# Kernel tuning notes

Measured on AMD Instinct MI355X. Metric: run time of the kernel, lower is better.

## Reference

```python
import math
import jax, jax.numpy as jnp
import numpy as np

H = 8  # num_heads

def _layernorm(x, scale, bias, eps=1e-5):
    m = x.mean(-1, keepdims=True)
    v = x.var(-1, keepdims=True)
    return (x - m) / jnp.sqrt(v + eps) * scale + bias

def setup_inputs() -> dict:
    key = jax.random.key(0)
    ks = jax.random.split(key, 12)
    B, C, P, D, G = 8, 32, 256, 256, 512
    n = jax.random.normal
    return {
        "qz": n(ks[0], (B, C, P, D), dtype=jnp.float32),
        "unary": n(ks[1], (B, C, P, D), dtype=jnp.float32),
        # per-sample condition-instantiated factors; scaled ~1/sqrt(D) so attn logits are sane
        "time_u": n(ks[2], (B, D, D), dtype=jnp.float32) * 0.06,
        "time_v": n(ks[3], (B, D, D), dtype=jnp.float32) * 0.06,
        "channel_u": n(ks[4], (B, D, D), dtype=jnp.float32) * 0.06,
        "channel_v": n(ks[5], (B, D, D), dtype=jnp.float32) * 0.06,
        "topic_binary": n(ks[6], (B, G, D), dtype=jnp.float32) * 0.02,
        "norm_scale": jnp.ones((D,), jnp.float32),
        "norm_bias": jnp.zeros((D,), jnp.float32),
        "gate_w": n(ks[7], (D, D), dtype=jnp.float32) * 0.02,
        "gate_b": jnp.zeros((D,), jnp.float32),
        "out_w1": n(ks[8], (D, D), dtype=jnp.float32) * 0.02,
        "out_b1": jnp.zeros((D,), jnp.float32),
        "out_w2": n(ks[9], (D, D), dtype=jnp.float32) * 0.02,
        "out_b2": jnp.zeros((D,), jnp.float32),
    }

def reference(qz, unary, time_u, time_v, channel_u, channel_v, topic_binary,
              norm_scale, norm_bias, gate_w, gate_b, out_w1, out_b1, out_w2, out_b2):
    B, C, P, D = qz.shape
    R = D // H
    inv_sqrt_r = 1.0 / math.sqrt(R)

    qz_n = _layernorm(qz, norm_scale, norm_bias)

    def heads(x, w):  # [B,C,P,D] x [B,D,D] -> [B,C,P,H,R]
        return jnp.einsum('bcpd,bod->bcpo', x, w).reshape(B, C, P, H, R)

    # --- time-factor message: attention over P within each (b, c, h) ---
    qu = heads(qz_n, time_u).transpose(0, 1, 3, 2, 4)   # [B,C,H,P,R]
    qv = heads(qz_n, time_v).transpose(0, 1, 3, 2, 4)
    attn_t = jax.nn.softmax(jnp.einsum('bchpr,bchqr->bchpq', qu, qv) * inv_sqrt_r, axis=-1)
    m_t = jnp.einsum('bchpq,bcqd->bchpd', attn_t, qz_n).mean(axis=2)  # [B,C,P,D]

    # --- channel-factor message: attention over C within each (b, p, h) ---
    qu = heads(qz_n, channel_u).transpose(0, 2, 3, 1, 4)  # [B,P,H,C,R]
    qv = heads(qz_n, channel_v).transpose(0, 2, 3, 1, 4)
    attn_c = jax.nn.softmax(jnp.einsum('bphcr,bphfr->bphcf', qu, qv) * inv_sqrt_r, axis=-1)
    qzp = qz_n.transpose(0, 2, 1, 3)                      # [B,P,C,D]
    m_c = jnp.einsum('bphcf,bpfd->bphcd', attn_c, qzp).mean(axis=2).transpose(0, 2, 1, 3)

    # --- topic-modeling binary factor with AbsNormalize (relu + L1-normalize) ---
    qg = jax.nn.relu(jnp.einsum('bcpd,bgd->bcpg', qz_n, topic_binary))
    qg = qg / jnp.maximum(qg.sum(axis=-1, keepdims=True), 1e-6)
    m_g = jnp.einsum('bcpg,bgd->bcpd', qg, topic_binary)

    # --- gated residual update ---
    gate = jax.nn.sigmoid(qz @ gate_w.T + gate_b)
    qz2 = gate * qz + (1.0 - gate) * (unary + m_t + m_c + m_g)

    # --- output MLP with shared LayerNorm ---
    h = _layernorm(qz2, norm_scale, norm_bias)
    h = jax.nn.gelu(h @ out_w1.T + out_b1, approximate=False) @ out_w2.T + out_b2
    return qz2 + h
```

## Files before the change

### kernel.cpp

```cpp
#include <hip/hip_runtime.h>
#include <math.h>

namespace {

constexpr float INV_SQRT_R = 0.17677669529663689f;

typedef __attribute__((ext_vector_type(8))) __bf16 bf16x8;
typedef __attribute__((ext_vector_type(4))) float f32x4;

static __device__ __forceinline__ f32x4 MF(bf16x8 a, bf16x8 b, f32x4 c) {
    return __builtin_amdgcn_mfma_f32_16x16x32_bf16(a, b, c, 0, 0, 0);
}

__global__ __launch_bounds__(256) void prep_kernel(
    const float* __restrict__ time_u, const float* __restrict__ time_v,
    const float* __restrict__ chan_u, const float* __restrict__ chan_v,
    const float* __restrict__ topic, const float* __restrict__ gate_w,
    const float* __restrict__ w1, const float* __restrict__ w2,
    __bf16* __restrict__ wtime, __bf16* __restrict__ wchan,
    __bf16* __restrict__ topicb, __bf16* __restrict__ topicTb,
    __bf16* __restrict__ gwb, __bf16* __restrict__ w1b, __bf16* __restrict__ w2b)
{
    __shared__ __bf16 tile[32][34];
    const int blk = blockIdx.x;
    const int t = threadIdx.x;
    if (blk < 2048) {
        const int q = blk >> 9, r = blk & 511;
        const float* src; __bf16* dst; int dstOff;
        if (q == 0)      { src = time_u; dst = wtime; dstOff = 0; }
        else if (q == 1) { src = time_v; dst = wtime; dstOff = 65536; }
        else if (q == 2) { src = chan_u; dst = wchan; dstOff = 0; }
        else             { src = chan_v; dst = wchan; dstOff = 65536; }
        int i = (r * 256 + t) * 4;
        float4 v = *(const float4*)(src + i);
        int o = (i >> 16) * 131072 + dstOff + (i & 65535);
        dst[o + 0] = (__bf16)v.x; dst[o + 1] = (__bf16)v.y;
        dst[o + 2] = (__bf16)v.z; dst[o + 3] = (__bf16)v.w;
    } else if (blk < 3072) {
        int i = ((blk - 2048) * 256 + t) * 4;
        float4 v = *(const float4*)(topic + i);
        topicb[i + 0] = (__bf16)v.x; topicb[i + 1] = (__bf16)v.y;
        topicb[i + 2] = (__bf16)v.z; topicb[i + 3] = (__bf16)v.w;
    } else if (blk < 4096) {
        const int idx = blk - 3072;
        const int r0 = (idx & 15) * 32;
        const int c0 = ((idx >> 4) & 7) * 32;
        const size_t bz = idx >> 7;
        const float* src = topic + bz * 131072;
        __bf16* dst = topicTb + bz * 131072;
        const int tx = t & 31, ty = t >> 5;
        #pragma unroll
        for (int i = 0; i < 32; i += 8)
            tile[ty + i][tx] = (__bf16)src[(size_t)(r0 + ty + i) * 256 + c0 + tx];
        __syncthreads();
        #pragma unroll
        for (int i = 0; i < 32; i += 8)
            dst[(size_t)(c0 + ty + i) * 512 + r0 + tx] = tile[tx][ty + i];
    } else {
        const int w = (blk - 4096) >> 6;
        const int r = (blk - 4096) & 63;
        const float* src = (w == 0) ? gate_w : ((w == 1) ? w1 : w2);
        __bf16* dst = (w == 0) ? gwb : ((w == 1) ? w1b : w2b);
        int i = (r * 256 + t) * 4;
        float4 v = *(const float4*)(src + i);
        dst[i + 0] = (__bf16)v.x; dst[i + 1] = (__bf16)v.y;
        dst[i + 2] = (__bf16)v.z; dst[i + 3] = (__bf16)v.w;
    }
}

__global__ __launch_bounds__(256) void ln_kernel(
    const float* __restrict__ x, const float* __restrict__ sc,
    const float* __restrict__ bi, __bf16* __restrict__ y)
{
    const size_t row = blockIdx.x;
    const int t = threadIdx.x;
    const float v = x[row * 256 + t];
    float s = v, s2 = v * v;
    #pragma unroll
    for (int o = 32; o > 0; o >>= 1) {
        s  += __shfl_xor(s, o);
        s2 += __shfl_xor(s2, o);
    }
    __shared__ float ps[4], ps2[4];
    if ((t & 63) == 0) { ps[t >> 6] = s; ps2[t >> 6] = s2; }
    __syncthreads();
    const float S  = ps[0] + ps[1] + ps[2] + ps[3];
    const float S2 = ps2[0] + ps2[1] + ps2[2] + ps2[3];
    const float mean = S * (1.0f / 256.0f);
    const float var  = S2 * (1.0f / 256.0f) - mean * mean;
    const float inv  = 1.0f / sqrtf(var + 1e-5f);
    y[row * 256 + t] = (__bf16)((v - mean) * inv * sc[t] + bi[t]);
}

__global__ __launch_bounds__(256) void tpose_bf_kernel(
    const __bf16* __restrict__ src, __bf16* __restrict__ dst, int R, int C)
{
    const size_t bz = blockIdx.z;
    src += bz * (size_t)R * C;
    dst += bz * (size_t)R * C;
    __shared__ __bf16 tile[32][34];
    const int r0 = blockIdx.x * 32, c0 = blockIdx.y * 32;
    const int tx = threadIdx.x & 31, ty = threadIdx.x >> 5;
    #pragma unroll
    for (int i = 0; i < 32; i += 8)
        tile[ty + i][tx] = src[(size_t)(r0 + ty + i) * C + c0 + tx];
    __syncthreads();
    #pragma unroll
    for (int i = 0; i < 32; i += 8)
        dst[(size_t)(c0 + ty + i) * R + r0 + tx] = tile[tx][ty + i];
}

__global__ __launch_bounds__(256) void mgemm_kernel(
    const __bf16* __restrict__ A, const __bf16* __restrict__ Bm, __bf16* __restrict__ Cout,
    int K, size_t aStride, size_t bStride,
    size_t s_b, size_t s_c, size_t s_p, size_t s_w, size_t s_h)
{
    const int bb = blockIdx.z;
    const int m0 = blockIdx.x * 64;
    const int n0 = blockIdx.y * 256;
    const __bf16* Ab = A + (size_t)bb * aStride;
    const __bf16* Bb = Bm + (size_t)bb * bStride;
    __shared__ __align__(16) __bf16 As[64][40];
    __shared__ __align__(16) __bf16 Bs[256][40];
    const int t = threadIdx.x;
    const int lane = t & 63;
    const int wid = t >> 6;
    const int l15 = lane & 15, lg = lane >> 4;

    f32x4 acc[4][4] = {};

    for (int k0 = 0; k0 < K; k0 += 32) {
        {
            const int row = t >> 2, k8 = (t & 3) << 3;
            *(bf16x8*)&As[row][k8] = *(const bf16x8*)(Ab + (size_t)(m0 + row) * K + k0 + k8);
        }
        #pragma unroll
        for (int s = 0; s < 4; ++s) {
            const int slot = s * 256 + t;
            const int row = slot >> 2, k8 = (slot & 3) << 3;
            *(bf16x8*)&Bs[row][k8] = *(const bf16x8*)(Bb + (size_t)(n0 + row) * K + k0 + k8);
        }
        __syncthreads();
        bf16x8 af[4], bfr[4];
        #pragma unroll
        for (int i = 0; i < 4; ++i)
            af[i] = *(const bf16x8*)&As[i * 16 + l15][lg * 8];
        #pragma unroll
        for (int j = 0; j < 4; ++j)
            bfr[j] = *(const bf16x8*)&Bs[wid * 64 + j * 16 + l15][lg * 8];
        #pragma unroll
        for (int i = 0; i < 4; ++i)
            #pragma unroll
            for (int j = 0; j < 4; ++j)
                acc[i][j] = MF(af[i], bfr[j], acc[i][j]);
        __syncthreads();
    }

    #pragma unroll
    for (int j = 0; j < 4; ++j) {
        const int n = n0 + wid * 64 + j * 16 + l15;
        const size_t offn = (size_t)(n >> 8) * s_w + (size_t)((n >> 5) & 7) * s_h + (n & 31);
        #pragma unroll
        for (int i = 0; i < 4; ++i) {
            #pragma unroll
            for (int r = 0; r < 4; ++r) {
                const int m = m0 + i * 16 + lg * 4 + r;
                const size_t off = (size_t)bb * s_b + (size_t)(m >> 8) * s_c
                                 + (size_t)(m & 255) * s_p + offn;
                Cout[off] = (__bf16)acc[i][j][r];
            }
        }
    }
}

__global__ __launch_bounds__(256) void time_attn_mt_kernel(
    const __bf16* __restrict__ qu, const __bf16* __restrict__ qv,
    const __bf16* __restrict__ qznT, __bf16* __restrict__ m_t)
{
    const int bc = blockIdx.x;
    const int p0 = blockIdx.y * 64;
    const __bf16* quB = qu + (size_t)bc * 65536;
    const __bf16* qvB = qv + (size_t)bc * 65536;
    const __bf16* BT  = qznT + (size_t)bc * 65536;
    __shared__ __align__(16) __bf16 R1[27136];
    __bf16* Us  = R1;
    __bf16* Vs  = R1 + 2560;
    __bf16* aL  = R1;
    __bf16* Bs2 = R1 + 16896;
    const int t = threadIdx.x;
    const int lane = t & 63;
    const int wid = t >> 6;
    const int l15 = lane & 15, lg = lane >> 4;

    f32x4 acc[16] = {};

    for (int h = 0; h < 8; ++h) {
        const __bf16* quH = quB + h * 8192;
        const __bf16* qvH = qvB + h * 8192;
        __syncthreads();
        {
            const int row = t >> 2, k8 = (t & 3) << 3;
            *(bf16x8*)&Us[row * 40 + k8] = *(const bf16x8*)(quH + (size_t)(p0 + row) * 32 + k8);
        }
        #pragma unroll
        for (int i = 0; i < 4; ++i) {
            const int slot = i * 256 + t;
            const int row = slot >> 2, k8 = (slot & 3) << 3;
            *(bf16x8*)&Vs[row * 40 + k8] = *(const bf16x8*)(qvH + (size_t)row * 32 + k8);
        }
        __syncthreads();

        f32x4 s[16];
        bf16x8 a = *(const bf16x8*)&Us[(wid * 16 + l15) * 40 + lg * 8];
        #pragma unroll
        for (int j = 0; j < 16; ++j) {
            bf16x8 bfr = *(const bf16x8*)&Vs[(j * 16 + l15) * 40 + lg * 8];
            s[j] = MF(a, bfr, (f32x4){0.f, 0.f, 0.f, 0.f});
        }

        #pragma unroll
        for (int r = 0; r < 4; ++r) {
            float e[16];
            float sum = 0.0f;
            #pragma unroll
            for (int j = 0; j < 16; ++j) {
                e[j] = __expf(s[j][r] * INV_SQRT_R);
                sum += e[j];
            }
            sum += __shfl_xor(sum, 1);
            sum += __shfl_xor(sum, 2);
            sum += __shfl_xor(sum, 4);
            sum += __shfl_xor(sum, 8);
            const float inv = 0.125f / sum;
            #pragma unroll
            for (int j = 0; j < 16; ++j) acc[j][r] += e[j] * inv;
        }
    }

    __syncthreads();
    #pragma unroll
    for (int r = 0; r < 4; ++r) {
        const int row = wid * 16 + lg * 4 + r;
        #pragma unroll
        for (int j = 0; j < 16; ++j)
            aL[row * 264 + j * 16 + l15] = (__bf16)acc[j][r];
    }
    __syncthreads();

    f32x4 acc2[4][4] = {};
    for (int k0 = 0; k0 < 256; k0 += 32) {
        #pragma unroll
        for (int s = 0; s < 4; ++s) {
            const int slot = s * 256 + t;
            const int row = slot >> 2, k8 = (slot & 3) << 3;
            *(bf16x8*)&Bs2[row * 40 + k8] = *(const bf16x8*)(BT + (size_t)row * 256 + k0 + k8);
        }
        __syncthreads();
        bf16x8 af[4], bfr[4];
        #pragma unroll
        for (int i = 0; i < 4; ++i)
            af[i] = *(const bf16x8*)&aL[(i * 16 + l15) * 264 + k0 + lg * 8];
        #pragma unroll
        for (int j = 0; j < 4; ++j)
            bfr[j] = *(const bf16x8*)&Bs2[(wid * 64 + j * 16 + l15) * 40 + lg * 8];
        #pragma unroll
        for (int i = 0; i < 4; ++i)
            #pragma unroll
            for (int j = 0; j < 4; ++j)
                acc2[i][j] = MF(af[i], bfr[j], acc2[i][j]);
        __syncthreads();
    }
    #pragma unroll
    for (int i = 0; i < 4; ++i)
        #pragma unroll
        for (int j = 0; j < 4; ++j) {
            const int d = wid * 64 + j * 16 + l15;
            #pragma unroll
            for (int r = 0; r < 4; ++r) {
                const int p = p0 + i * 16 + lg * 4 + r;
                m_t[(size_t)bc * 65536 + (size_t)p * 256 + d] = (__bf16)acc2[i][j][r];
            }
        }
}

__global__ __launch_bounds__(256) void chan_fused_kernel(
    const __bf16* __restrict__ quc, const __bf16* __restrict__ qvc,
    const __bf16* __restrict__ qzn, __bf16* __restrict__ m_c)
{
    const int bp = blockIdx.x;
    const int b = bp >> 8, p = bp & 255;
    const __bf16* quB = quc + (size_t)bp * 8192;
    const __bf16* qvB = qvc + (size_t)bp * 8192;
    __shared__ __align__(16) __bf16 QU[20480];
    __shared__ float ab[32 * 33];
    __bf16* qus = QU;
    __bf16* qvs = QU + 10240;
    const int t = threadIdx.x;

    float btr[32];
    #pragma unroll
    for (int f = 0; f < 32; ++f)
        btr[f] = (float)qzn[((size_t)(b * 32 + f) * 256 + p) * 256 + t];

    #pragma unroll
    for (int i = 0; i < 4; ++i) {
        int fi = i * 256 + t;
        int e = fi << 3;
        int h = e >> 10, cc = (e >> 5) & 31, r = e & 31;
        int base = (h * 32 + cc) * 40 + r;
        *(bf16x8*)&qus[base] = *(const bf16x8*)(quB + e);
        *(bf16x8*)&qvs[base] = *(const bf16x8*)(qvB + e);
    }
    __syncthreads();
    const int c = t >> 3, j = t & 7;
    float acc[4] = {0.f, 0.f, 0.f, 0.f};
    for (int h = 0; h < 8; ++h) {
        float qur[32];
        #pragma unroll
        for (int u = 0; u < 4; ++u) {
            bf16x8 q8 = *(const bf16x8*)&qus[(h * 32 + c) * 40 + u * 8];
            #pragma unroll
            for (int e2 = 0; e2 < 8; ++e2) qur[u * 8 + e2] = (float)q8[e2];
        }
        float s[4];
        #pragma unroll
        for (int jj = 0; jj < 4; ++jj) {
            int f = j * 4 + jj;
            float a = 0.f;
            #pragma unroll
            for (int u = 0; u < 4; ++u) {
                bf16x8 v8 = *(const bf16x8*)&qvs[(h * 32 + f) * 40 + u * 8];
                #pragma unroll
                for (int e2 = 0; e2 < 8; ++e2) a += qur[u * 8 + e2] * (float)v8[e2];
            }
            s[jj] = a * INV_SQRT_R;
        }
        float mx = fmaxf(fmaxf(s[0], s[1]), fmaxf(s[2], s[3]));
        mx = fmaxf(mx, __shfl_xor(mx, 1));
        mx = fmaxf(mx, __shfl_xor(mx, 2));
        mx = fmaxf(mx, __shfl_xor(mx, 4));
        float e0x = __expf(s[0] - mx), e1x = __expf(s[1] - mx);
        float e2x = __expf(s[2] - mx), e3x = __expf(s[3] - mx);
        float sum = e0x + e1x + e2x + e3x;
        sum += __shfl_xor(sum, 1);
        sum += __shfl_xor(sum, 2);
        sum += __shfl_xor(sum, 4);
        float inv = 0.125f / sum;
        acc[0] += e0x * inv; acc[1] += e1x * inv; acc[2] += e2x * inv; acc[3] += e3x * inv;
    }
    #pragma unroll
    for (int jj = 0; jj < 4; ++jj) ab[c * 33 + j * 4 + jj] = acc[jj];
    __syncthreads();
    #pragma unroll 2
    for (int c2 = 0; c2 < 32; c2 += 2) {
        float a0 = 0.f, a1 = 0.f;
        #pragma unroll
        for (int f = 0; f < 32; ++f) {
            float v = btr[f];
            a0 += ab[c2 * 33 + f] * v;
            a1 += ab[(c2 + 1) * 33 + f] * v;
        }
        size_t off = ((size_t)(b * 32 + c2) * 256 + p) * 256 + t;
        m_c[off] = (__bf16)a0;
        m_c[off + 65536] = (__bf16)a1;
    }
}

__global__ __launch_bounds__(256, 2) void topic_fused_kernel(
    const __bf16* __restrict__ qzn, const __bf16* __restrict__ topicb,
    const __bf16* __restrict__ topicTb, __bf16* __restrict__ m_g)
{
    const int bb = blockIdx.z;
    const int m0 = blockIdx.x * 32;
    const __bf16* Ab = qzn + (size_t)bb * 2097152;
    const __bf16* B1 = topicb + (size_t)bb * 131072;
    const __bf16* B2 = topicTb + (size_t)bb * 131072;
    __shared__ __align__(16) __bf16 As[32][40];
    __shared__ __align__(16) __bf16 Bs[512][40];
    __shared__ __align__(16) __bf16 Ps[32][520];
    __shared__ float rsInv[32];
    const int t = threadIdx.x;
    const int lane = t & 63, wid = t >> 6;
    const int l15 = lane & 15, lg = lane >> 4;

    f32x4 acc[2][8] = {};
    for (int k0 = 0; k0 < 256; k0 += 32) {
        if (t < 128) {
            const int row = t >> 2, k8 = (t & 3) << 3;
            *(bf16x8*)&As[row][k8] = *(const bf16x8*)(Ab + (size_t)(m0 + row) * 256 + k0 + k8);
        }
        #pragma unroll
        for (int s = 0; s < 8; ++s) {
            const int slot = s * 256 + t;
            const int row = slot >> 2, k8 = (slot & 3) << 3;
            *(bf16x8*)&Bs[row][k8] = *(const bf16x8*)(B1 + (size_t)row * 256 + k0 + k8);
        }
        __syncthreads();
        bf16x8 af0 = *(const bf16x8*)&As[l15][lg * 8];
        bf16x8 af1 = *(const bf16x8*)&As[16 + l15][lg * 8];
        #pragma unroll
        for (int j = 0; j < 8; ++j) {
            bf16x8 b8 = *(const bf16x8*)&Bs[wid * 128 + j * 16 + l15][lg * 8];
            acc[0][j] = MF(af0, b8, acc[0][j]);
            acc[1][j] = MF(af1, b8, acc[1][j]);
        }
        __syncthreads();
    }
    #pragma unroll
    for (int i = 0; i < 2; ++i)
        #pragma unroll
        for (int j = 0; j < 8; ++j) {
            const int n = wid * 128 + j * 16 + l15;
            #pragma unroll
            for (int r = 0; r < 4; ++r)
                Ps[i * 16 + lg * 4 + r][n] = (__bf16)fmaxf(acc[i][j][r], 0.0f);
        }
    __syncthreads();
    {
        const int row = t >> 3, seg = t & 7;
        float s = 0.0f;
        #pragma unroll
        for (int u = 0; u < 8; ++u) {
            bf16x8 v = *(const bf16x8*)&Ps[row][seg * 64 + u * 8];
            #pragma unroll
            for (int e = 0; e < 8; ++e) s += (float)v[e];
        }
        s += __shfl_xor(s, 1);
        s += __shfl_xor(s, 2);
        s += __shfl_xor(s, 4);
        if (seg == 0) rsInv[row] = 1.0f / fmaxf(s, 1e-6f);
    }
    __syncthreads();
    f32x4 acc2[2][4] = {};
    for (int k0 = 0; k0 < 512; k0 += 32) {
        #pragma unroll
        for (int s = 0; s < 4; ++s) {
            const int slot = s * 256 + t;
            const int row = slot >> 2, k8 = (slot & 3) << 3;
            *(bf16x8*)&Bs[row][k8] = *(const bf16x8*)(B2 + (size_t)row * 512 + k0 + k8);
        }
        __syncthreads();
        bf16x8 af0 = *(const bf16x8*)&Ps[l15][k0 + lg * 8];
        bf16x8 af1 = *(const bf16x8*)&Ps[16 + l15][k0 + lg * 8];
        #pragma unroll
        for (int j = 0; j < 4; ++j) {
            bf16x8 b8 = *(const bf16x8*)&Bs[wid * 64 + j * 16 + l15][lg * 8];
            acc2[0][j] = MF(af0, b8, acc2[0][j]);
            acc2[1][j] = MF(af1, b8, acc2[1][j]);
        }
        __syncthreads();
    }
    #pragma unroll
    for (int i = 0; i < 2; ++i)
        #pragma unroll
        for (int j = 0; j < 4; ++j) {
            const int n = wid * 64 + j * 16 + l15;
            #pragma unroll
            for (int r = 0; r < 4; ++r) {
                const int ml = i * 16 + lg * 4 + r;
                m_g[(size_t)bb * 2097152 + (size_t)(m0 + ml) * 256 + n]
                    = (__bf16)(acc2[i][j][r] * rsInv[ml]);
            }
        }
}

__global__ __launch_bounds__(256) void mega_kernel(
    const float* __restrict__ qz, const float* __restrict__ unary,
    const __bf16* __restrict__ m_t, const __bf16* __restrict__ m_c,
    const __bf16* __restrict__ m_g,
    const __bf16* __restrict__ gwb, const float* __restrict__ gate_b,
    const __bf16* __restrict__ w1b, const float* __restrict__ b1,
    const __bf16* __restrict__ w2b, const float* __restrict__ b2,
    const float* __restrict__ nsc, const float* __restrict__ nbi,
    float* __restrict__ outp)
{
    const int m0 = blockIdx.x * 64;
    __shared__ __align__(16) __bf16 Bs[256][40];
    __shared__ __align__(16) __bf16 hL[64][264];
    float* lnp = (float*)Bs;
    const int t = threadIdx.x;
    const int lane = t & 63, wid = t >> 6;
    const int l15 = lane & 15, lg = lane >> 4;

    #pragma unroll
    for (int s = 0; s < 8; ++s) {
        const int slot = s * 256 + t;
        const int row = slot >> 5;
        const int k8 = (slot & 31) << 3;
        const float* src = qz + (size_t)(m0 + row) * 256 + k8;
        float4 v0 = *(const float4*)src;
        float4 v1 = *(const float4*)(src + 4);
        bf16x8 pk;
        pk[0] = (__bf16)v0.x; pk[1] = (__bf16)v0.y; pk[2] = (__bf16)v0.z; pk[3] = (__bf16)v0.w;
        pk[4] = (__bf16)v1.x; pk[5] = (__bf16)v1.y; pk[6] = (__bf16)v1.z; pk[7] = (__bf16)v1.w;
        *(bf16x8*)&hL[row][k8] = pk;
    }

    f32x4 acc[4][4] = {};
    for (int k0 = 0; k0 < 256; k0 += 32) {
        #pragma unroll
        for (int s = 0; s < 4; ++s) {
            const int slot = s * 256 + t;
            const int row = slot >> 2, k8 = (slot & 3) << 3;
            *(bf16x8*)&Bs[row][k8] = *(const bf16x8*)(gwb + (size_t)row * 256 + k0 + k8);
        }
        __syncthreads();
        bf16x8 af[4], bfr[4];
        #pragma unroll
        for (int i = 0; i < 4; ++i) af[i] = *(const bf16x8*)&hL[i * 16 + l15][k0 + lg * 8];
        #pragma unroll
        for (int j = 0; j < 4; ++j) bfr[j] = *(const bf16x8*)&Bs[wid * 64 + j * 16 + l15][lg * 8];
        #pragma unroll
        for (int i = 0; i < 4; ++i)
            #pragma unroll
            for (int j = 0; j < 4; ++j)
                acc[i][j] = MF(af[i], bfr[j], acc[i][j]);
        __syncthreads();
    }

    f32x4 z2[4][4];
    #pragma unroll
    for (int i = 0; i < 4; ++i) {
        #pragma unroll
        for (int r = 0; r < 4; ++r) {
            const int rr = i * 16 + lg * 4 + r;
            float s = 0.0f, s2 = 0.0f;
            #pragma unroll
            for (int j = 0; j < 4; ++j) {
                const int n = wid * 64 + j * 16 + l15;
                const size_t off = (size_t)(m0 + rr) * 256 + n;
                float g = 1.0f / (1.0f + __expf(-(acc[i][j][r] + gate_b[n])));
                float rest = unary[off] + (float)m_t[off] + (float)m_c[off] + (float)m_g[off];
                float v = g * (float)hL[rr][n] + (1.0f - g) * rest;
                z2[i][j][r] = v;
                s += v; s2 += v * v;
            }
            s  += __shfl_xor(s, 1);  s  += __shfl_xor(s, 2);
            s  += __shfl_xor(s, 4);  s  += __shfl_xor(s, 8);
            s2 += __shfl_xor(s2, 1); s2 += __shfl_xor(s2, 2);
            s2 += __shfl_xor(s2, 4); s2 += __shfl_xor(s2, 8);
            if (l15 == 0) {
                lnp[rr * 8 + wid * 2 + 0] = s;
                lnp[rr * 8 + wid * 2 + 1] = s2;
            }
        }
    }
    __syncthreads();
    #pragma unroll
    for (int i = 0; i < 4; ++i) {
        #pragma unroll
        for (int r = 0; r < 4; ++r) {
            const int rr = i * 16 + lg * 4 + r;
            float S  = lnp[rr * 8 + 0] + lnp[rr * 8 + 2] + lnp[rr * 8 + 4] + lnp[rr * 8 + 6];
            float S2 = lnp[rr * 8 + 1] + lnp[rr * 8 + 3] + lnp[rr * 8 + 5] + lnp[rr * 8 + 7];
            float mean = S * (1.0f / 256.0f);
            float var  = S2 * (1.0f / 256.0f) - mean * mean;
            float inv  = 1.0f / sqrtf(var + 1e-5f);
            #pragma unroll
            for (int j = 0; j < 4; ++j) {
                const int n = wid * 64 + j * 16 + l15;
                hL[rr][n] = (__bf16)((z2[i][j][r] - mean) * inv * nsc[n] + nbi[n]);
            }
        }
    }
    __syncthreads();

    f32x4 acc2[4][4] = {};
    for (int k0 = 0; k0 < 256; k0 += 32) {
        #pragma unroll
        for (int s = 0; s < 4; ++s) {
            const int slot = s * 256 + t;
            const int row = slot >> 2, k8 = (slot & 3) << 3;
            *(bf16x8*)&Bs[row][k8] = *(const bf16x8*)(w1b + (size_t)row * 256 + k0 + k8);
        }
        __syncthreads();
        bf16x8 af[4], bfr[4];
        #pragma unroll
        for (int i = 0; i < 4; ++i) af[i] = *(const bf16x8*)&hL[i * 16 + l15][k0 + lg * 8];
        #pragma unroll
        for (int j = 0; j < 4; ++j) bfr[j] = *(const bf16x8*)&Bs[wid * 64 + j * 16 + l15][lg * 8];
        #pragma unroll
        for (int i = 0; i < 4; ++i)
            #pragma unroll
            for (int j = 0; j < 4; ++j)
                acc2[i][j] = MF(af[i], bfr[j], acc2[i][j]);
        __syncthreads();
    }
    #pragma unroll
    for (int i = 0; i < 4; ++i)
        #pragma unroll
        for (int j = 0; j < 4; ++j) {
            const int n = wid * 64 + j * 16 + l15;
            const float bn = b1[n];
            #pragma unroll
            for (int r = 0; r < 4; ++r) {
                float x = acc2[i][j][r] + bn;
                hL[i * 16 + lg * 4 + r][n] = (__bf16)(0.5f * x * (1.0f + erff(x * 0.7071067811865475f)));
            }
        }
    __syncthreads();

    f32x4 acc3[4][4] = {};
    for (int k0 = 0; k0 < 256; k0 += 32) {
        #pragma unroll
        for (int s = 0; s < 4; ++s) {
            const int slot = s * 256 + t;
            const int row = slot >> 2, k8 = (slot & 3) << 3;
            *(bf16x8*)&Bs[row][k8] = *(const bf16x8*)(w2b + (size_t)row * 256 + k0 + k8);
        }
        __syncthreads();
        bf16x8 af[4], bfr[4];
        #pragma unroll
        for (int i = 0; i < 4; ++i) af[i] = *(const bf16x8*)&hL[i * 16 + l15][k0 + lg * 8];
        #pragma unroll
        for (int j = 0; j < 4; ++j) bfr[j] = *(const bf16x8*)&Bs[wid * 64 + j * 16 + l15][lg * 8];
        #pragma unroll
        for (int i = 0; i < 4; ++i)
            #pragma unroll
            for (int j = 0; j < 4; ++j)
                acc3[i][j] = MF(af[i], bfr[j], acc3[i][j]);
        __syncthreads();
    }
    #pragma unroll
    for (int i = 0; i < 4; ++i)
        #pragma unroll
        for (int j = 0; j < 4; ++j) {
            const int n = wid * 64 + j * 16 + l15;
            const float bn = b2[n];
            #pragma unroll
            for (int r = 0; r < 4; ++r) {
                const size_t off = (size_t)(m0 + i * 16 + lg * 4 + r) * 256 + n;
                outp[off] = z2[i][j][r] + acc3[i][j][r] + bn;
            }
        }
}

}

extern "C" void kernel_launch(void* const* d_in, const int* in_sizes, int n_in,
                              void* d_out, int out_size, void* d_ws, size_t ws_size,
                              hipStream_t stream)
{
    (void)in_sizes; (void)n_in; (void)out_size; (void)ws_size;
    const float* qz     = (const float*)d_in[0];
    const float* unary  = (const float*)d_in[1];
    const float* time_u = (const float*)d_in[2];
    const float* time_v = (const float*)d_in[3];
    const float* chan_u = (const float*)d_in[4];
    const float* chan_v = (const float*)d_in[5];
    const float* topic  = (const float*)d_in[6];
    const float* nsc    = (const float*)d_in[7];
    const float* nbi    = (const float*)d_in[8];
    const float* gate_w = (const float*)d_in[9];
    const float* gate_b = (const float*)d_in[10];
    const float* w1     = (const float*)d_in[11];
    const float* b1     = (const float*)d_in[12];
    const float* w2     = (const float*)d_in[13];
    const float* b2     = (const float*)d_in[14];

    char* base = (char*)d_ws;
    __bf16* qzn_b  = (__bf16*)base;
    __bf16* pool   = (__bf16*)(base + (32ull << 20));
    __bf16* wtime  = pool;
    __bf16* wchan  = pool + 1048576;
    __bf16* topicb = pool + 2097152;
    __bf16* topicTb= pool + 3145728;
    __bf16* gwb    = pool + 4194304;
    __bf16* w1b    = pool + 4259840;
    __bf16* w2b    = pool + 4325376;
    __bf16* Blo    = (__bf16*)(base + (64ull << 20));
    __bf16* Bhi    = (__bf16*)(base + (96ull << 20));
    __bf16* qu_t   = Blo;
    __bf16* qv_t   = Bhi;
    __bf16* qu_c   = Blo;
    __bf16* qv_c   = Bhi;
    __bf16* m_g    = Blo;
    __bf16* qznT   = (__bf16*)(base + (128ull << 20));
    __bf16* m_c    = qznT;
    __bf16* m_t    = (__bf16*)(base + (160ull << 20));
    float*  OUTF   = (float*)d_out;

    dim3 blk(256);

    prep_kernel<<<4288, blk, 0, stream>>>(
        time_u, time_v, chan_u, chan_v, topic, gate_w, w1, w2,
        wtime, wchan, topicb, topicTb, gwb, w1b, w2b);

    ln_kernel<<<65536, blk, 0, stream>>>(qz, nsc, nbi, qzn_b);
    tpose_bf_kernel<<<dim3(8, 8, 256), blk, 0, stream>>>(qzn_b, qznT, 256, 256);

    mgemm_kernel<<<dim3(128, 2, 8), blk, 0, stream>>>(
        qzn_b, wtime, qu_t, 256, 2097152, 131072,
        2097152, 65536, 32, 16777216, 8192);

    time_attn_mt_kernel<<<dim3(256, 4), blk, 0, stream>>>(qu_t, qv_t, qznT, m_t);

    mgemm_kernel<<<dim3(128, 2, 8), blk, 0, stream>>>(
        qzn_b, wchan, qu_c, 256, 2097152, 131072,
        2097152, 32, 8192, 16777216, 1024);

    chan_fused_kernel<<<2048, blk, 0, stream>>>(qu_c, qv_c, qzn_b, m_c);

    topic_fused_kernel<<<dim3(256, 1, 8), blk, 0, stream>>>(qzn_b, topicb, topicTb, m_g);

    mega_kernel<<<1024, blk, 0, stream>>>(
        qz, unary, m_t, m_c, m_g,
        gwb, gate_b, w1b, b1, w2b, b2, nsc, nbi, OUTF);
}
```

Before: 523.0 us.

## Pre-tile B operands into fragment-friendly layout and read them directly from global

The prep and transpose kernels now write weights, topic matrices and the transposed qz_n into a k-block-major layout (32-wide k chunks, rows contiguous). The GEMM loops in the time-attention, topic and mega kernels then load B fragments straight from global memory as 16-byte vectors, with no LDS staging and no per-k-step barriers. The topic kernel also stages its full A tile once and drops its 2-blocks-per-SM launch bound. This cuts LDS traffic and synchronisation, but makes MFMA operand fetches depend on global/L2 latency with no explicit prefetch.

```diff
diff --git a/kernel.cpp b/kernel.cpp
--- a/kernel.cpp
+++ b/kernel.cpp
@@ -11,6 +11,7 @@
 static __device__ __forceinline__ f32x4 MF(bf16x8 a, bf16x8 b, f32x4 c) {
     return __builtin_amdgcn_mfma_f32_16x16x32_bf16(a, b, c, 0, 0, 0);
 }
+
 
 __global__ __launch_bounds__(256) void prep_kernel(
     const float* __restrict__ time_u, const float* __restrict__ time_v,
@@ -18,8 +19,8 @@
     const float* __restrict__ topic, const float* __restrict__ gate_w,
     const float* __restrict__ w1, const float* __restrict__ w2,
     __bf16* __restrict__ wtime, __bf16* __restrict__ wchan,
-    __bf16* __restrict__ topicb, __bf16* __restrict__ topicTb,
-    __bf16* __restrict__ gwb, __bf16* __restrict__ w1b, __bf16* __restrict__ w2b)
+    __bf16* __restrict__ topicFb, __bf16* __restrict__ topicTFb,
+    __bf16* __restrict__ gwF, __bf16* __restrict__ w1F, __bf16* __restrict__ w2F)
 {
     __shared__ __bf16 tile[32][34];
     const int blk = blockIdx.x;
@@ -39,15 +40,17 @@
     } else if (blk < 3072) {
         int i = ((blk - 2048) * 256 + t) * 4;
         float4 v = *(const float4*)(topic + i);
-        topicb[i + 0] = (__bf16)v.x; topicb[i + 1] = (__bf16)v.y;
-        topicb[i + 2] = (__bf16)v.z; topicb[i + 3] = (__bf16)v.w;
+        const int b = i >> 17, rem = i & 131071;
+        const int g = rem >> 8, d = rem & 255;
+        __bf16* dst = topicFb + (size_t)b * 131072 + (d >> 5) * 16384 + g * 32 + (d & 31);
+        dst[0] = (__bf16)v.x; dst[1] = (__bf16)v.y; dst[2] = (__bf16)v.z; dst[3] = (__bf16)v.w;
     } else if (blk < 4096) {
         const int idx = blk - 3072;
         const int r0 = (idx & 15) * 32;
         const int c0 = ((idx >> 4) & 7) * 32;
         const size_t bz = idx >> 7;
         const float* src = topic + bz * 131072;
-        __bf16* dst = topicTb + bz * 131072;
+        __bf16* dst = topicTFb + bz * 131072;
         const int tx = t & 31, ty = t >> 5;
         #pragma unroll
         for (int i = 0; i < 32; i += 8)
@@ -55,16 +58,17 @@
         __syncthreads();
         #pragma unroll
         for (int i = 0; i < 32; i += 8)
-            dst[(size_t)(c0 + ty + i) * 512 + r0 + tx] = tile[tx][ty + i];
+            dst[(r0 >> 5) * 8192 + (c0 + ty + i) * 32 + tx] = tile[tx][ty + i];
     } else {
         const int w = (blk - 4096) >> 6;
         const int r = (blk - 4096) & 63;
         const float* src = (w == 0) ? gate_w : ((w == 1) ? w1 : w2);
-        __bf16* dst = (w == 0) ? gwb : ((w == 1) ? w1b : w2b);
+        __bf16* dstB = (w == 0) ? gwF : ((w == 1) ? w1F : w2F);
         int i = (r * 256 + t) * 4;
         float4 v = *(const float4*)(src + i);
-        dst[i + 0] = (__bf16)v.x; dst[i + 1] = (__bf16)v.y;
-        dst[i + 2] = (__bf16)v.z; dst[i + 3] = (__bf16)v.w;
+        const int n = i >> 8, k = i & 255;
+        __bf16* dst = dstB + (k >> 5) * 8192 + n * 32 + (k & 31);
+        dst[0] = (__bf16)v.x; dst[1] = (__bf16)v.y; dst[2] = (__bf16)v.z; dst[3] = (__bf16)v.w;
     }
 }
 
@@ -92,22 +96,22 @@
     y[row * 256 + t] = (__bf16)((v - mean) * inv * sc[t] + bi[t]);
 }
 
-__global__ __launch_bounds__(256) void tpose_bf_kernel(
-    const __bf16* __restrict__ src, __bf16* __restrict__ dst, int R, int C)
+__global__ __launch_bounds__(256) void tpose_frag_kernel(
+    const __bf16* __restrict__ src, __bf16* __restrict__ dst)
 {
     const size_t bz = blockIdx.z;
-    src += bz * (size_t)R * C;
-    dst += bz * (size_t)R * C;
+    src += bz * 65536;
+    dst += bz * 65536;
     __shared__ __bf16 tile[32][34];
     const int r0 = blockIdx.x * 32, c0 = blockIdx.y * 32;
     const int tx = threadIdx.x & 31, ty = threadIdx.x >> 5;
     #pragma unroll
     for (int i = 0; i < 32; i += 8)
-        tile[ty + i][tx] = src[(size_t)(r0 + ty + i) * C + c0 + tx];
+        tile[ty + i][tx] = src[(size_t)(r0 + ty + i) * 256 + c0 + tx];
     __syncthreads();
     #pragma unroll
     for (int i = 0; i < 32; i += 8)
-        dst[(size_t)(c0 + ty + i) * R + r0 + tx] = tile[tx][ty + i];
+        dst[(r0 >> 5) * 8192 + (c0 + ty + i) * 32 + tx] = tile[tx][ty + i];
 }
 
 __global__ __launch_bounds__(256) void mgemm_kernel(
@@ -175,18 +179,17 @@
 
 __global__ __launch_bounds__(256) void time_attn_mt_kernel(
     const __bf16* __restrict__ qu, const __bf16* __restrict__ qv,
-    const __bf16* __restrict__ qznT, __bf16* __restrict__ m_t)
+    const __bf16* __restrict__ qznTF, __bf16* __restrict__ m_t)
 {
     const int bc = blockIdx.x;
     const int p0 = blockIdx.y * 64;
     const __bf16* quB = qu + (size_t)bc * 65536;
     const __bf16* qvB = qv + (size_t)bc * 65536;
-    const __bf16* BT  = qznT + (size_t)bc * 65536;
-    __shared__ __align__(16) __bf16 R1[27136];
+    const __bf16* BTF = qznTF + (size_t)bc * 65536;
+    __shared__ __align__(16) __bf16 R1[16896];
     __bf16* Us  = R1;
     __bf16* Vs  = R1 + 2560;
     __bf16* aL  = R1;
-    __bf16* Bs2 = R1 + 16896;
     const int t = threadIdx.x;
     const int lane = t & 63;
     const int wid = t >> 6;
@@ -248,27 +251,20 @@
     __syncthreads();
 
     f32x4 acc2[4][4] = {};
+    #pragma unroll
     for (int k0 = 0; k0 < 256; k0 += 32) {
-        #pragma unroll
-        for (int s = 0; s < 4; ++s) {
-            const int slot = s * 256 + t;
-            const int row = slot >> 2, k8 = (slot & 3) << 3;
-            *(bf16x8*)&Bs2[row * 40 + k8] = *(const bf16x8*)(BT + (size_t)row * 256 + k0 + k8);
-        }
-        __syncthreads();
         bf16x8 af[4], bfr[4];
         #pragma unroll
         for (int i = 0; i < 4; ++i)
             af[i] = *(const bf16x8*)&aL[(i * 16 + l15) * 264 + k0 + lg * 8];
         #pragma unroll
         for (int j = 0; j < 4; ++j)
-            bfr[j] = *(const bf16x8*)&Bs2[(wid * 64 + j * 16 + l15) * 40 + lg * 8];
+            bfr[j] = *(const bf16x8*)(BTF + (k0 >> 5) * 8192 + (wid * 64 + j * 16 + l15) * 32 + lg * 8);
         #pragma unroll
         for (int i = 0; i < 4; ++i)
             #pragma unroll
             for (int j = 0; j < 4; ++j)
                 acc2[i][j] = MF(af[i], bfr[j], acc2[i][j]);
-        __syncthreads();
     }
     #pragma unroll
     for (int i = 0; i < 4; ++i)
@@ -366,45 +362,41 @@
     }
 }
 
-__global__ __launch_bounds__(256, 2) void topic_fused_kernel(
-    const __bf16* __restrict__ qzn, const __bf16* __restrict__ topicb,
-    const __bf16* __restrict__ topicTb, __bf16* __restrict__ m_g)
+__global__ __launch_bounds__(256) void topic_fused_kernel(
+    const __bf16* __restrict__ qzn, const __bf16* __restrict__ topicFb,
+    const __bf16* __restrict__ topicTFb, __bf16* __restrict__ m_g)
 {
     const int bb = blockIdx.z;
     const int m0 = blockIdx.x * 32;
     const __bf16* Ab = qzn + (size_t)bb * 2097152;
-    const __bf16* B1 = topicb + (size_t)bb * 131072;
-    const __bf16* B2 = topicTb + (size_t)bb * 131072;
-    __shared__ __align__(16) __bf16 As[32][40];
-    __shared__ __align__(16) __bf16 Bs[512][40];
+    const __bf16* B1 = topicFb + (size_t)bb * 131072;
+    const __bf16* B2 = topicTFb + (size_t)bb * 131072;
+    __shared__ __align__(16) __bf16 As[32][264];
     __shared__ __align__(16) __bf16 Ps[32][520];
     __shared__ float rsInv[32];
     const int t = threadIdx.x;
     const int lane = t & 63, wid = t >> 6;
     const int l15 = lane & 15, lg = lane >> 4;
 
+    #pragma unroll
+    for (int s = 0; s < 4; ++s) {
+        const int slot = s * 256 + t;
+        const int row = slot >> 5, k8 = (slot & 31) << 3;
+        *(bf16x8*)&As[row][k8] = *(const bf16x8*)(Ab + (size_t)(m0 + row) * 256 + k8);
+    }
+    __syncthreads();
+
     f32x4 acc[2][8] = {};
+    #pragma unroll
     for (int k0 = 0; k0 < 256; k0 += 32) {
-        if (t < 128) {
-            const int row = t >> 2, k8 = (t & 3) << 3;
-            *(bf16x8*)&As[row][k8] = *(const bf16x8*)(Ab + (size_t)(m0 + row) * 256 + k0 + k8);
-        }
-        #pragma unroll
-        for (int s = 0; s < 8; ++s) {
-            const int slot = s * 256 + t;
-            const int row = slot >> 2, k8 = (slot & 3) << 3;
-            *(bf16x8*)&Bs[row][k8] = *(const bf16x8*)(B1 + (size_t)row * 256 + k0 + k8);
-        }
-        __syncthreads();
-        bf16x8 af0 = *(const bf16x8*)&As[l15][lg * 8];
-        bf16x8 af1 = *(const bf16x8*)&As[16 + l15][lg * 8];
+        bf16x8 af0 = *(const bf16x8*)&As[l15][k0 + lg * 8];
+        bf16x8 af1 = *(const bf16x8*)&As[16 + l15][k0 + lg * 8];
         #pragma unroll
         for (int j = 0; j < 8; ++j) {
-            bf16x8 b8 = *(const bf16x8*)&Bs[wid * 128 + j * 16 + l15][lg * 8];
+            bf16x8 b8 = *(const bf16x8*)(B1 + (k0 >> 5) * 16384 + (wid * 128 + j * 16 + l15) * 32 + lg * 8);
             acc[0][j] = MF(af0, b8, acc[0][j]);
             acc[1][j] = MF(af1, b8, acc[1][j]);
         }
-        __syncthreads();
     }
     #pragma unroll
     for (int i = 0; i < 2; ++i)
@@ -432,23 +424,16 @@
     }
     __syncthreads();
     f32x4 acc2[2][4] = {};
+    #pragma unroll
     for (int k0 = 0; k0 < 512; k0 += 32) {
-        #pragma unroll
-        for (int s = 0; s < 4; ++s) {
-            const int slot = s * 256 + t;
-            const int row = slot >> 2, k8 = (slot & 3) << 3;
-            *(bf16x8*)&Bs[row][k8] = *(const bf16x8*)(B2 + (size_t)row * 512 + k0 + k8);
-        }
-        __syncthreads();
         bf16x8 af0 = *(const bf16x8*)&Ps[l15][k0 + lg * 8];
         bf16x8 af1 = *(const bf16x8*)&Ps[16 + l15][k0 + lg * 8];
         #pragma unroll
         for (int j = 0; j < 4; ++j) {
-            bf16x8 b8 = *(const bf16x8*)&Bs[wid * 64 + j * 16 + l15][lg * 8];
+            bf16x8 b8 = *(const bf16x8*)(B2 + (k0 >> 5) * 8192 + (wid * 64 + j * 16 + l15) * 32 + lg * 8);
             acc2[0][j] = MF(af0, b8, acc2[0][j]);
             acc2[1][j] = MF(af1, b8, acc2[1][j]);
         }
-        __syncthreads();
     }
     #pragma unroll
     for (int i = 0; i < 2; ++i)
@@ -468,16 +453,15 @@
     const float* __restrict__ qz, const float* __restrict__ unary,
     const __bf16* __restrict__ m_t, const __bf16* __restrict__ m_c,
     const __bf16* __restrict__ m_g,
-    const __bf16* __restrict__ gwb, const float* __restrict__ gate_b,
-    const __bf16* __restrict__ w1b, const float* __restrict__ b1,
-    const __bf16* __restrict__ w2b, const float* __restrict__ b2,
+    const __bf16* __restrict__ gwF, const float* __restrict__ gate_b,
+    const __bf16* __restrict__ w1F, const float* __restrict__ b1,
+    const __bf16* __restrict__ w2F, const float* __restrict__ b2,
     const float* __restrict__ nsc, const float* __restrict__ nbi,
     float* __restrict__ outp)
 {
     const int m0 = blockIdx.x * 64;
-    __shared__ __align__(16) __bf16 Bs[256][40];
     __shared__ __align__(16) __bf16 hL[64][264];
-    float* lnp = (float*)Bs;
+    __shared__ float lnp[64][8];
     const int t = threadIdx.x;
     const int lane = t & 63, wid = t >> 6;
     const int l15 = lane & 15, lg = lane >> 4;
@@ -495,27 +479,22 @@
         pk[4] = (__bf16)v1.x; pk[5] = (__bf16)v1.y; pk[6] = (__bf16)v1.z; pk[7] = (__bf16)v1.w;
         *(bf16x8*)&hL[row][k8] = pk;
     }
+    __syncthreads();
 
     f32x4 acc[4][4] = {};
+    #pragma unroll
     for (int k0 = 0; k0 < 256; k0 += 32) {
-        #pragma unroll
-        for (int s = 0; s < 4; ++s) {
-            const int slot = s * 256 + t;
-            const int row = slot >> 2, k8 = (slot & 3) << 3;
-            *(bf16x8*)&Bs[row][k8] = *(const bf16x8*)(gwb + (size_t)row * 256 + k0 + k8);
-        }
-        __syncthreads();
         bf16x8 af[4], bfr[4];
         #pragma unroll
         for (int i = 0; i < 4; ++i) af[i] = *(const bf16x8*)&hL[i * 16 + l15][k0 + lg * 8];
         #pragma unroll
-        for (int j = 0; j < 4; ++j) bfr[j] = *(const bf16x8*)&Bs[wid * 64 + j * 16 + l15][lg * 8];
+        for (int j = 0; j < 4; ++j)
+            bfr[j] = *(const bf16x8*)(gwF + (k0 >> 5) * 8192 + (wid * 64 + j * 16 + l15) * 32 + lg * 8);
         #pragma unroll
         for (int i = 0; i < 4; ++i)
             #pragma unroll
             for (int j = 0; j < 4; ++j)
                 acc[i][j] = MF(af[i], bfr[j], acc[i][j]);
-        __syncthreads();
     }
 
     f32x4 z2[4][4];
@@ -540,8 +519,8 @@
             s2 += __shfl_xor(s2, 1); s2 += __shfl_xor(s2, 2);
             s2 += __shfl_xor(s2, 4); s2 += __shfl_xor(s2, 8);
             if (l15 == 0) {
-                lnp[rr * 8 + wid * 2 + 0] = s;
-                lnp[rr * 8 + wid * 2 + 1] = s2;
+                lnp[rr][wid * 2 + 0] = s;
+                lnp[rr][wid * 2 + 1] = s2;
             }
         }
     }
@@ -551,8 +530,8 @@
         #pragma unroll
         for (int r = 0; r < 4; ++r) {
             const int rr = i * 16 + lg * 4 + r;
-            float S  = lnp[rr * 8 + 0] + lnp[rr * 8 + 2] + lnp[rr * 8 + 4] + lnp[rr * 8 + 6];
-            float S2 = lnp[rr * 8 + 1] + lnp[rr * 8 + 3] + lnp[rr * 8 + 5] + lnp[rr * 8 + 7];
+            float S  = lnp[rr][0] + lnp[rr][2] + lnp[rr][4] + lnp[rr][6];
+            float S2 = lnp[rr][1] + lnp[rr][3] + lnp[rr][5] + lnp[rr][7];
             float mean = S * (1.0f / 256.0f);
             float var  = S2 * (1.0f / 256.0f) - mean * mean;
             float inv  = 1.0f / sqrtf(var + 1e-5f);
@@ -566,26 +545,21 @@
     __syncthreads();
 
     f32x4 acc2[4][4] = {};
+    #pragma unroll
     for (int k0 = 0; k0 < 256; k0 += 32) {
-        #pragma unroll
-        for (int s = 0; s < 4; ++s) {
-            const int slot = s * 256 + t;
-            const int row = slot >> 2, k8 = (slot & 3) << 3;
-            *(bf16x8*)&Bs[row][k8] = *(const bf16x8*)(w1b + (size_t)row * 256 + k0 + k8);
-        }
-        __syncthreads();
         bf16x8 af[4], bfr[4];
         #pragma unroll
         for (int i = 0; i < 4; ++i) af[i] = *(const bf16x8*)&hL[i * 16 + l15][k0 + lg * 8];
         #pragma unroll
-        for (int j = 0; j < 4; ++j) bfr[j] = *(const bf16x8*)&Bs[wid * 64 + j * 16 + l15][lg * 8];
+        for (int j = 0; j < 4; ++j)
+            bfr[j] = *(const bf16x8*)(w1F + (k0 >> 5) * 8192 + (wid * 64 + j * 16 + l15) * 32 + lg * 8);
         #pragma unroll
         for (int i = 0; i < 4; ++i)
             #pragma unroll
             for (int j = 0; j < 4; ++j)
                 acc2[i][j] = MF(af[i], bfr[j], acc2[i][j]);
-        __syncthreads();
-    }
+    }
+    __syncthreads();
     #pragma unroll
     for (int i = 0; i < 4; ++i)
         #pragma unroll
@@ -601,25 +575,19 @@
     __syncthreads();
 
     f32x4 acc3[4][4] = {};
+    #pragma unroll
     for (int k0 = 0; k0 < 256; k0 += 32) {
-        #pragma unroll
-        for (int s = 0; s < 4; ++s) {
-            const int slot = s * 256 + t;
-            const int row = slot >> 2, k8 = (slot & 3) << 3;
-            *(bf16x8*)&Bs[row][k8] = *(const bf16x8*)(w2b + (size_t)row * 256 + k0 + k8);
-        }
-        __syncthreads();
         bf16x8 af[4], bfr[4];
         #pragma unroll
         for (int i = 0; i < 4; ++i) af[i] = *(const bf16x8*)&hL[i * 16 + l15][k0 + lg * 8];
         #pragma unroll
-        for (int j = 0; j < 4; ++j) bfr[j] = *(const bf16x8*)&Bs[wid * 64 + j * 16 + l15][lg * 8];
+        for (int j = 0; j < 4; ++j)
+            bfr[j] = *(const bf16x8*)(w2F + (k0 >> 5) * 8192 + (wid * 64 + j * 16 + l15) * 32 + lg * 8);
         #pragma unroll
         for (int i = 0; i < 4; ++i)
             #pragma unroll
             for (int j = 0; j < 4; ++j)
                 acc3[i][j] = MF(af[i], bfr[j], acc3[i][j]);
-        __syncthreads();
     }
     #pragma unroll
     for (int i = 0; i < 4; ++i)
@@ -663,11 +631,11 @@
     __bf16* pool   = (__bf16*)(base + (32ull << 20));
     __bf16* wtime  = pool;
     __bf16* wchan  = pool + 1048576;
-    __bf16* topicb = pool + 2097152;
-    __bf16* topicTb= pool + 3145728;
-    __bf16* gwb    = pool + 4194304;
-    __bf16* w1b    = pool + 4259840;
-    __bf16* w2b    = pool + 4325376;
+    __bf16* topicFb = pool + 2097152;
+    __bf16* topicTFb= pool + 3145728;
+    __bf16* gwF    = pool + 4194304;
+    __bf16* w1F    = pool + 4259840;
+    __bf16* w2F    = pool + 4325376;
     __bf16* Blo    = (__bf16*)(base + (64ull << 20));
     __bf16* Bhi    = (__bf16*)(base + (96ull << 20));
     __bf16* qu_t   = Blo;
@@ -675,8 +643,8 @@
     __bf16* qu_c   = Blo;
     __bf16* qv_c   = Bhi;
     __bf16* m_g    = Blo;
-    __bf16* qznT   = (__bf16*)(base + (128ull << 20));
-    __bf16* m_c    = qznT;
+    __bf16* qznTF  = (__bf16*)(base + (128ull << 20));
+    __bf16* m_c    = qznTF;
     __bf16* m_t    = (__bf16*)(base + (160ull << 20));
     float*  OUTF   = (float*)d_out;
 
@@ -684,16 +652,16 @@
 
     prep_kernel<<<4288, blk, 0, stream>>>(
         time_u, time_v, chan_u, chan_v, topic, gate_w, w1, w2,
-        wtime, wchan, topicb, topicTb, gwb, w1b, w2b);
+        wtime, wchan, topicFb, topicTFb, gwF, w1F, w2F);
 
     ln_kernel<<<65536, blk, 0, stream>>>(qz, nsc, nbi, qzn_b);
-    tpose_bf_kernel<<<dim3(8, 8, 256), blk, 0, stream>>>(qzn_b, qznT, 256, 256);
+    tpose_frag_kernel<<<dim3(8, 8, 256), blk, 0, stream>>>(qzn_b, qznTF);
 
     mgemm_kernel<<<dim3(128, 2, 8), blk, 0, stream>>>(
         qzn_b, wtime, qu_t, 256, 2097152, 131072,
         2097152, 65536, 32, 16777216, 8192);
 
-    time_attn_mt_kernel<<<dim3(256, 4), blk, 0, stream>>>(qu_t, qv_t, qznT, m_t);
+    time_attn_mt_kernel<<<dim3(256, 4), blk, 0, stream>>>(qu_t, qv_t, qznTF, m_t);
 
     mgemm_kernel<<<dim3(128, 2, 8), blk, 0, stream>>>(
         qzn_b, wchan, qu_c, 256, 2097152, 131072,
@@ -701,9 +669,9 @@
 
     chan_fused_kernel<<<2048, blk, 0, stream>>>(qu_c, qv_c, qzn_b, m_c);
 
-    topic_fused_kernel<<<dim3(256, 1, 8), blk, 0, stream>>>(qzn_b, topicb, topicTb, m_g);
+    topic_fused_kernel<<<dim3(256, 1, 8), blk, 0, stream>>>(qzn_b, topicFb, topicTFb, m_g);
 
     mega_kernel<<<1024, blk, 0, stream>>>(
         qz, unary, m_t, m_c, m_g,
-        gwb, gate_b, w1b, b1, w2b, b2, nsc, nbi, OUTF);
-}
+        gwF, gate_b, w1F, b1, w2F, b2, nsc, nbi, OUTF);
+}
```

After: 530.6 us. No clear change (+1.5%).
